# Kernel tuning notes

Measured on AMD Instinct MI355X. Metric: run time of the kernel, lower is better.

The kernel has to match this reference:

```python
import jax, jax.numpy as jnp
import numpy as np

N_QUBITS = 4
DIM = 16  # 2**4 amplitudes
VOCAB = 40
SEQ = 1048576

# PennyLane default.qubit: wire 0 is the most-significant bit of the basis index.
_BITS = np.array([[(b >> (N_QUBITS - 1 - q)) & 1 for q in range(N_QUBITS)]
                  for b in range(DIM)], dtype=np.int32)          # [16, 4]
_POPCNT = _BITS.sum(axis=1)                                      # [16] int
_ZSIGN = (1 - 2 * _BITS).astype(np.float32)                      # [16, 4], +1 for |0>, -1 for |1>

def _cnot_perm(c, t):
    # basis permutation of CNOT(control=c, target=t); it is an involution
    idx = np.arange(DIM)
    ctrl = (idx >> (N_QUBITS - 1 - c)) & 1
    flipped = idx ^ (1 << (N_QUBITS - 1 - t))
    return np.where(ctrl == 1, flipped, idx)

_PERMS = [_cnot_perm(i, i + 1) for i in range(N_QUBITS - 1)]  # CNOT(0,1),(1,2),(2,3)


def setup_inputs() -> dict:
    key = jax.random.key(0)
    k1, k2, k3 = jax.random.split(key, 3)
    x = jax.random.uniform(k1, (1, SEQ), dtype=jnp.float32)
    q_weights = 0.01 * jax.random.normal(k2, (N_QUBITS,), dtype=jnp.float32)
    fc_weight = jax.random.normal(k3, (VOCAB, N_QUBITS), dtype=jnp.float32) / jnp.sqrt(4.0)
    fc_bias = jnp.zeros((VOCAB,), dtype=jnp.float32)
    return {"x": x, "q_weights": q_weights, "fc_weight": fc_weight, "fc_bias": fc_bias}


def reference(x, q_weights, fc_weight, fc_bias):
    theta = x[0]                      # [S] per-token angle, same on all 4 wires
    c = jnp.cos(theta * 0.5)
    s = jnp.sin(theta * 0.5)
    one = jnp.ones_like(c)
    # powers c^k, s^k for k=0..4 (avoids pow-grad issues at 0)
    cpow = jnp.stack([one, c, c * c, c * c * c, c * c * c * c], axis=-1)  # [S,5]
    spow = jnp.stack([one, s, s * s, s * s * s, s * s * s * s], axis=-1)  # [S,5]
    # product state of RY(theta)|0> on each wire: amp_b = c^(4-popcnt) * s^popcnt
    state = cpow[:, N_QUBITS - _POPCNT] * spow[:, _POPCNT]               # [S,16] real
    # apply the CNOT chain (basis permutations)
    for p in _PERMS:
        state = state[:, p]
    # RZ(w_q) on each wire contributes phase exp(-i*w_q*z_q/2)
    zs = jnp.asarray(_ZSIGN)                                              # [16,4]
    phase = jnp.exp(-0.5j * (zs @ q_weights.astype(jnp.float32)))         # [16] complex
    psi = state.astype(jnp.complex64) * phase                             # [S,16]
    probs = jnp.real(psi * jnp.conj(psi))                                 # [S,16]
    expvals = probs @ zs                                                  # [S,4] <Z_q>
    return expvals @ fc_weight.T + fc_bias                                # [S,VOCAB]
```

## Files before the change

### kernel.cpp

```cpp
#include <hip/hip_runtime.h>

#define THREADS 320
#define ROWS_PER_BLOCK 512
#define F4_PER_BLOCK 5120
#define ITERS 16

typedef float f32x4 __attribute__((ext_vector_type(4)));

__global__ __launch_bounds__(THREADS) void sqm_kernel(
    const float* __restrict__ x,
    const float* __restrict__ fcw,
    const float* __restrict__ fcb,
    float* __restrict__ out)
{
    __shared__ __align__(16) float sP[5][40];
    __shared__ float sS[ROWS_PER_BLOCK];

    const int t = threadIdx.x;

    if (t < 40) {
        const f32x4 w = *reinterpret_cast<const f32x4*>(&fcw[t * 4]);
        const float b = fcb[t];
        sP[0][t] = w.x + w.y + w.z + w.w + b;
        sP[1][t] = -2.f*w.x - 4.f*w.y - 6.f*w.z - 8.f*w.w;
        sP[2][t] =           4.f*w.y + 12.f*w.z + 24.f*w.w;
        sP[3][t] =                     -8.f*w.z - 32.f*w.w;
        sP[4][t] =                                16.f*w.w;
    }

    const int rowBase = blockIdx.x * ROWS_PER_BLOCK;
    {
        const float th0 = x[rowBase + t];
        sS[t] = 0.5f - 0.5f * __cosf(th0);
        if (t < ROWS_PER_BLOCK - THREADS) {
            const float th1 = x[rowBase + THREADS + t];
            sS[THREADS + t] = 0.5f - 0.5f * __cosf(th1);
        }
    }
    __syncthreads();

    const int m4 = (t % 10) * 4;
    const f32x4 p0 = *reinterpret_cast<const f32x4*>(&sP[0][m4]);
    const f32x4 p1 = *reinterpret_cast<const f32x4*>(&sP[1][m4]);
    const f32x4 p2 = *reinterpret_cast<const f32x4*>(&sP[2][m4]);
    const f32x4 p3 = *reinterpret_cast<const f32x4*>(&sP[3][m4]);
    const f32x4 p4 = *reinterpret_cast<const f32x4*>(&sP[4][m4]);

    const int rloc0 = t / 10;
    float Sv[ITERS];
    #pragma unroll
    for (int it = 0; it < ITERS; ++it)
        Sv[it] = sS[rloc0 + it * 32];

    f32x4* __restrict__ out4 = reinterpret_cast<f32x4*>(out);
    const long long blockF4 = (long long)blockIdx.x * F4_PER_BLOCK + t;
    #pragma unroll
    for (int it = 0; it < ITERS; ++it) {
        const float S = Sv[it];
        f32x4 r = p4;
        r = r * S + p3;
        r = r * S + p2;
        r = r * S + p1;
        r = r * S + p0;
        out4[blockF4 + it * THREADS] = r;
    }
}

extern "C" void kernel_launch(void* const* d_in, const int* in_sizes, int n_in,
                              void* d_out, int out_size, void* d_ws, size_t ws_size,
                              hipStream_t stream) {
    const float* x   = (const float*)d_in[0];
    const float* fcw = (const float*)d_in[2];
    const float* fcb = (const float*)d_in[3];
    float* out = (float*)d_out;
    const int n = in_sizes[0];
    const int grid = n / ROWS_PER_BLOCK;
    hipLaunchKernelGGL(sqm_kernel, dim3(grid), dim3(THREADS), 0, stream,
                       x, fcw, fcb, out);
}
```

Baseline: 169.0 us.

## Split angle preprocessing into separate kernel and drop shared memory staging

Moves the per-token cos computation into a separate vectorized prep kernel that writes S to workspace. The main kernel then reads S straight from global memory, computes the polynomial coefficients per thread in registers with no shared memory or barrier, and doubles the rows per block. This removes the __syncthreads and LDS staging from the write-bound kernel, at the cost of a second launch and an extra round trip of the S array through global memory.

```diff
diff --git a/kernel.cpp b/kernel.cpp
--- a/kernel.cpp
+++ b/kernel.cpp
@@ -1,68 +1,63 @@
 #include <hip/hip_runtime.h>
 
 #define THREADS 320
-#define ROWS_PER_BLOCK 512
-#define F4_PER_BLOCK 5120
-#define ITERS 16
+#define ROWS_PER_BLOCK 1024
+#define F4_PER_BLOCK 10240
+#define ITERS 32
 
 typedef float f32x4 __attribute__((ext_vector_type(4)));
 
-__global__ __launch_bounds__(THREADS) void sqm_kernel(
-    const float* __restrict__ x,
+__global__ __launch_bounds__(256) void sqm_prep(
+    const float* __restrict__ x, float* __restrict__ Sg)
+{
+    const int i = (blockIdx.x * 256 + threadIdx.x) * 4;
+    const f32x4 v = *reinterpret_cast<const f32x4*>(x + i);
+    f32x4 s;
+    s.x = 0.5f - 0.5f * __cosf(v.x);
+    s.y = 0.5f - 0.5f * __cosf(v.y);
+    s.z = 0.5f - 0.5f * __cosf(v.z);
+    s.w = 0.5f - 0.5f * __cosf(v.w);
+    *reinterpret_cast<f32x4*>(Sg + i) = s;
+}
+
+__global__ __launch_bounds__(THREADS) void sqm_main(
+    const float* __restrict__ Sg,
     const float* __restrict__ fcw,
     const float* __restrict__ fcb,
     float* __restrict__ out)
 {
-    __shared__ __align__(16) float sP[5][40];
-    __shared__ float sS[ROWS_PER_BLOCK];
+    const int t = threadIdx.x;
+    const int m = t % 10;
 
-    const int t = threadIdx.x;
+    float P0[4], P1[4], P2[4], P3[4], P4[4];
+    #pragma unroll
+    for (int c = 0; c < 4; ++c) {
+        const f32x4 w = *reinterpret_cast<const f32x4*>(&fcw[(4*m + c) * 4]);
+        const float b = fcb[4*m + c];
+        P0[c] = w.x + w.y + w.z + w.w + b;
+        P1[c] = -2.f*w.x - 4.f*w.y - 6.f*w.z - 8.f*w.w;
+        P2[c] =           4.f*w.y + 12.f*w.z + 24.f*w.w;
+        P3[c] =                     -8.f*w.z - 32.f*w.w;
+        P4[c] =                                16.f*w.w;
+    }
+    const f32x4 p0 = {P0[0], P0[1], P0[2], P0[3]};
+    const f32x4 p1 = {P1[0], P1[1], P1[2], P1[3]};
+    const f32x4 p2 = {P2[0], P2[1], P2[2], P2[3]};
+    const f32x4 p3 = {P3[0], P3[1], P3[2], P3[3]};
+    const f32x4 p4 = {P4[0], P4[1], P4[2], P4[3]};
 
-    if (t < 40) {
-        const f32x4 w = *reinterpret_cast<const f32x4*>(&fcw[t * 4]);
-        const float b = fcb[t];
-        sP[0][t] = w.x + w.y + w.z + w.w + b;
-        sP[1][t] = -2.f*w.x - 4.f*w.y - 6.f*w.z - 8.f*w.w;
-        sP[2][t] =           4.f*w.y + 12.f*w.z + 24.f*w.w;
-        sP[3][t] =                     -8.f*w.z - 32.f*w.w;
-        sP[4][t] =                                16.f*w.w;
-    }
-
-    const int rowBase = blockIdx.x * ROWS_PER_BLOCK;
-    {
-        const float th0 = x[rowBase + t];
-        sS[t] = 0.5f - 0.5f * __cosf(th0);
-        if (t < ROWS_PER_BLOCK - THREADS) {
-            const float th1 = x[rowBase + THREADS + t];
-            sS[THREADS + t] = 0.5f - 0.5f * __cosf(th1);
-        }
-    }
-    __syncthreads();
-
-    const int m4 = (t % 10) * 4;
-    const f32x4 p0 = *reinterpret_cast<const f32x4*>(&sP[0][m4]);
-    const f32x4 p1 = *reinterpret_cast<const f32x4*>(&sP[1][m4]);
-    const f32x4 p2 = *reinterpret_cast<const f32x4*>(&sP[2][m4]);
-    const f32x4 p3 = *reinterpret_cast<const f32x4*>(&sP[3][m4]);
-    const f32x4 p4 = *reinterpret_cast<const f32x4*>(&sP[4][m4]);
-
-    const int rloc0 = t / 10;
-    float Sv[ITERS];
-    #pragma unroll
-    for (int it = 0; it < ITERS; ++it)
-        Sv[it] = sS[rloc0 + it * 32];
-
-    f32x4* __restrict__ out4 = reinterpret_cast<f32x4*>(out);
-    const long long blockF4 = (long long)blockIdx.x * F4_PER_BLOCK + t;
-    #pragma unroll
+    const float* Sb = Sg + blockIdx.x * ROWS_PER_BLOCK + t / 10;
+    f32x4* __restrict__ outp = reinterpret_cast<f32x4*>(out)
+                             + (long long)blockIdx.x * F4_PER_BLOCK + t;
+    #pragma unroll 8
     for (int it = 0; it < ITERS; ++it) {
-        const float S = Sv[it];
+        const float S = Sb[it * 32];
         f32x4 r = p4;
         r = r * S + p3;
         r = r * S + p2;
         r = r * S + p1;
         r = r * S + p0;
-        out4[blockF4 + it * THREADS] = r;
+        outp[it * THREADS] = r;
     }
 }
 
@@ -73,8 +68,10 @@
     const float* fcw = (const float*)d_in[2];
     const float* fcb = (const float*)d_in[3];
     float* out = (float*)d_out;
+    float* Sg  = (float*)d_ws;
     const int n = in_sizes[0];
-    const int grid = n / ROWS_PER_BLOCK;
-    hipLaunchKernelGGL(sqm_kernel, dim3(grid), dim3(THREADS), 0, stream,
-                       x, fcw, fcb, out);
+
+    hipLaunchKernelGGL(sqm_prep, dim3(n / 1024), dim3(256), 0, stream, x, Sg);
+    hipLaunchKernelGGL(sqm_main, dim3(n / ROWS_PER_BLOCK), dim3(THREADS), 0,
+                       stream, Sg, fcw, fcb, out);
 }
```

New measurement: 173.3 us. 2.6% more time.
